# Kernel optimization log

Measured on AMD Instinct MI355X. Metric: run time of the kernel, lower is better.

## Reference

```python
import jax, jax.numpy as jnp
import numpy as np

B, T, C = 4, 2048, 1024


def wkv(k, v, w, u, reverse):
    """RWKV WKV scan with running-max stabilization.
    k, v: [B, T, C]; w, u: [C]. Returns y: [B, T, C]."""
    def step(carry, kv):
        num, den, mx = carry          # each [B, C]
        k_t, v_t = kv                 # each [B, C]
        ku = k_t + u
        m = jnp.maximum(mx, ku)
        e1 = jnp.exp(mx - m)
        e2 = jnp.exp(ku - m)
        y = (e1 * num + e2 * v_t) / (e1 * den + e2)
        # state update with decay w
        mw = mx + w
        mn = jnp.maximum(mw, k_t)
        e1s = jnp.exp(mw - mn)
        e2s = jnp.exp(k_t - mn)
        return (e1s * num + e2s * v_t, e1s * den + e2s, mn), y

    z = jnp.zeros_like(k[:, 0])
    init = (z, z, jnp.full_like(z, -1e38))
    ks = jnp.swapaxes(k, 0, 1)  # [T, B, C]
    vs = jnp.swapaxes(v, 0, 1)
    _, ys = jax.lax.scan(step, init, (ks, vs), reverse=reverse)
    return jnp.swapaxes(ys, 0, 1)


def setup_inputs() -> dict:
    key = jax.random.key(0)
    k1, k2, k3, k4, k5, k6, k7 = jax.random.split(key, 7)
    x = jax.random.normal(k1, (B, T, C), dtype=jnp.float32)
    rkv_w = jax.random.normal(k2, (6 * C, C), dtype=jnp.float32) / np.sqrt(C)
    out_w = jax.random.normal(k3, (C, 2 * C), dtype=jnp.float32) / np.sqrt(2 * C)
    time_decay = jax.random.uniform(k4, (C,), jnp.float32, -6.0, -5.0)
    time_first = jax.random.uniform(k5, (C,), jnp.float32, -3.0, 0.0)
    time_decay_rev = jax.random.uniform(k6, (C,), jnp.float32, -6.0, -5.0)
    time_first_rev = jax.random.uniform(k7, (C,), jnp.float32, -3.0, 0.0)
    return {"x": x, "rkv_w": rkv_w, "out_w": out_w,
            "time_decay": time_decay, "time_first": time_first,
            "time_decay_rev": time_decay_rev, "time_first_rev": time_first_rev}


def reference(x, rkv_w, out_w, time_decay, time_first, time_decay_rev, time_first_rev):
    b, t, c = x.shape
    rkv = jnp.einsum('btc,dc->btd', x, rkv_w).reshape(b, t, 2, 3, c)
    r_f, k_f, v_f = rkv[:, :, 0, 0], rkv[:, :, 0, 1], rkv[:, :, 0, 2]
    r_b, k_b, v_b = rkv[:, :, 1, 0], rkv[:, :, 1, 1], rkv[:, :, 1, 2]
    out_f = jax.nn.sigmoid(r_f) * wkv(k_f, v_f, -jnp.exp(time_decay), time_first, False)
    out_b = jax.nn.sigmoid(r_b) * wkv(k_b, v_b, -jnp.exp(time_decay_rev), time_first_rev, True)
    out_cat = jnp.concatenate([out_f, out_b], axis=-1)  # [B, T, 2C]
    return jnp.einsum('btd,cd->btc', out_cat, out_w)
```

## Files before the change

kernel.cpp:

```cpp
#include <hip/hip_runtime.h>
#include <cstdint>
#include <cstddef>

#define Bdim 4
#define Tdim 2048
#define Cdim 1024

#define SEG  16
#define CHB  32
#define LSEG (Tdim / SEG)

typedef __attribute__((ext_vector_type(8))) short bf16x8;
typedef __attribute__((ext_vector_type(4))) float f32x4;

__device__ __forceinline__ unsigned short f2bf(float f) {
    unsigned int u = __float_as_uint(f);
    u += 0x7fffu + ((u >> 16) & 1u);
    return (unsigned short)(u >> 16);
}
__device__ __forceinline__ float bf2f(unsigned short h) {
    return __uint_as_float((unsigned int)h << 16);
}

__device__ __forceinline__ void gload_lds16(const void* g, void* l) {
    __builtin_amdgcn_global_load_lds(
        (const __attribute__((address_space(1))) unsigned int*)g,
        (__attribute__((address_space(3))) unsigned int*)l,
        16, 0, 0);
}

__global__ __launch_bounds__(256) void cast_f32_bf16(
    const float* __restrict__ in, unsigned short* __restrict__ out, int n4)
{
    int i = blockIdx.x * 256 + threadIdx.x;
    if (i >= n4) return;
    float4 v = ((const float4*)in)[i];
    ushort4 o;
    o.x = f2bf(v.x); o.y = f2bf(v.y); o.z = f2bf(v.z); o.w = f2bf(v.w);
    ((ushort4*)out)[i] = o;
}

__device__ __forceinline__ void stage_half(
    const unsigned short* __restrict__ G, int row0, int K, int elemoff,
    char* slot, int wave, int lane)
{
    const int sl = (lane & 3) ^ ((lane >> 3) & 3);
    const unsigned short* gp = G + (size_t)(row0 + wave * 16 + (lane >> 2)) * K
                                 + elemoff + sl * 8;
    gload_lds16(gp, slot + wave * 1024);
    gload_lds16(gp + (size_t)128 * K, slot + 8192 + wave * 1024);
}

#define GPHASE(D, KH, MH, SG, SROW0, SOFF, SSLOT, VM)                          \
  {                                                                            \
    const char* As_ = ldsb + (D)*32768 + (KH)*16384;                           \
    const char* Bs_ = ldsb + 65536 + (D)*32768 + (KH)*16384;                   \
    bf16x8 a_[4], b_[4];                                                       \
    _Pragma("unroll")                                                          \
    for (int i_ = 0; i_ < 4; ++i_)                                             \
      a_[i_] = *(const bf16x8*)(As_ + (wm*128 + ((MH)*4+i_)*16 + fr)*64 + cswz);\
    _Pragma("unroll")                                                          \
    for (int j_ = 0; j_ < 4; ++j_)                                             \
      b_[j_] = *(const bf16x8*)(Bs_ + (wn*64 + j_*16 + fr)*64 + cswz);         \
    stage_half(SG, SROW0, K, SOFF, SSLOT, wave, lane);                         \
    __builtin_amdgcn_s_barrier();                                              \
    __builtin_amdgcn_sched_barrier(0);                                         \
    __builtin_amdgcn_s_setprio(1);                                             \
    _Pragma("unroll")                                                          \
    for (int i_ = 0; i_ < 4; ++i_)                                             \
      _Pragma("unroll")                                                        \
      for (int j_ = 0; j_ < 4; ++j_)                                           \
        acc[(MH)*4+i_][j_] = __builtin_amdgcn_mfma_f32_16x16x32_bf16(          \
            a_[i_], b_[j_], acc[(MH)*4+i_][j_], 0, 0, 0);                      \
    __builtin_amdgcn_s_setprio(0);                                             \
    if (VM) { asm volatile("s_waitcnt vmcnt(8)" ::: "memory"); }               \
    __builtin_amdgcn_s_barrier();                                              \
    __builtin_amdgcn_sched_barrier(0);                                         \
  }

__global__ __launch_bounds__(512, 2) void gemm_bf16_nt_256_obf(
    const unsigned short* __restrict__ A, const unsigned short* __restrict__ B,
    unsigned short* __restrict__ C, int M, int N, int K, int gx)
{
    __shared__ char ldsbuf[131072];
    char* ldsb = ldsbuf;

    const int tid  = threadIdx.x;
    const int wave = tid >> 6;
    const int lane = tid & 63;
    const int wm = wave >> 2;
    const int wn = wave & 3;
    const int fr = lane & 15;
    const int cswz = (((lane >> 4) ^ ((fr >> 1) & 3)) << 4);

    const int nwg = gridDim.x;
    const int cpx = nwg >> 3;
    const int b0  = blockIdx.x;
    const int swz = (b0 & 7) * cpx + (b0 >> 3);
    const int bx  = swz % gx;
    const int by  = swz / gx;
    const int m0 = by * 256;
    const int n0 = bx * 256;

    const int NKT = K >> 6;
    const int NI  = K >> 7;

    f32x4 acc[8][4] = {};

    stage_half(A, m0, K, 0,  ldsb + 0,             wave, lane);
    stage_half(B, n0, K, 0,  ldsb + 65536,         wave, lane);
    stage_half(A, m0, K, 32, ldsb + 16384,         wave, lane);
    stage_half(B, n0, K, 32, ldsb + 65536 + 16384, wave, lane);
    stage_half(A, m0, K, 64, ldsb + 32768,         wave, lane);
    stage_half(B, n0, K, 64, ldsb + 65536 + 32768, wave, lane);
    asm volatile("s_waitcnt vmcnt(8)" ::: "memory");
    __builtin_amdgcn_s_barrier();
    __builtin_amdgcn_sched_barrier(0);

    for (int i = 0; i < NI; ++i) {
        const int k1e = (2 * i + 1) * 64;
        int k2 = 2 * i + 2; if (k2 >= NKT) k2 = NKT - 1;
        int k3 = 2 * i + 3; if (k3 >= NKT) k3 = NKT - 1;
        const int k2e = k2 * 64, k3e = k3 * 64;

        GPHASE(0, 0, 0, A, m0, k1e + 32, ldsb + 32768 + 16384,         0)
        GPHASE(0, 0, 1, B, n0, k1e + 32, ldsb + 65536 + 32768 + 16384, 1)
        GPHASE(0, 1, 0, A, m0, k2e,      ldsb + 0,                     0)
        GPHASE(0, 1, 1, B, n0, k2e,      ldsb + 65536,                 1)
        GPHASE(1, 0, 0, A, m0, k2e + 32, ldsb + 16384,                 0)
        GPHASE(1, 0, 1, B, n0, k2e + 32, ldsb + 65536 + 16384,         1)
        GPHASE(1, 1, 0, A, m0, k3e,      ldsb + 32768,                 0)
        GPHASE(1, 1, 1, B, n0, k3e,      ldsb + 65536 + 32768,         1)
    }

    #pragma unroll
    for (int mi = 0; mi < 8; ++mi) {
        const int row = m0 + wm * 128 + mi * 16 + (lane >> 4) * 4;
        #pragma unroll
        for (int nj = 0; nj < 4; ++nj) {
            const int col = n0 + wn * 64 + nj * 16 + fr;
            #pragma unroll
            for (int r = 0; r < 4; ++r)
                C[(size_t)(row + r) * N + col] = f2bf(acc[mi][nj][r]);
        }
    }
}

__global__ __launch_bounds__(256) void gemm_bf16_nt(
    const unsigned short* __restrict__ A, const unsigned short* __restrict__ B,
    float* __restrict__ C, int M, int N, int K)
{
    __shared__ unsigned short As[128 * 32];
    __shared__ unsigned short Bs[128 * 32];

    const int tid  = threadIdx.x;
    const int wave = tid >> 6;
    const int lane = tid & 63;
    const int m0 = blockIdx.y * 128;
    const int n0 = blockIdx.x * 128;
    const int wr = wave >> 1, wc = wave & 1;

    const int srow = tid >> 2;
    const int scol = (tid & 3) * 8;
    const unsigned short* Ag = A + (size_t)(m0 + srow) * K + scol;
    const unsigned short* Bg = B + (size_t)(n0 + srow) * K + scol;
    char* AsW = (char*)As + wave * 1024;
    char* BsW = (char*)Bs + wave * 1024;

    f32x4 acc[4][4] = {};

    const int fr = lane & 15;
    const int fk = (lane >> 4) * 8;

    for (int k0 = 0; k0 < K; k0 += 32) {
        gload_lds16(Ag + k0,                  AsW);
        gload_lds16(Ag + k0 + (size_t)64 * K, AsW + 4096);
        gload_lds16(Bg + k0,                  BsW);
        gload_lds16(Bg + k0 + (size_t)64 * K, BsW + 4096);
        __syncthreads();

        bf16x8 af[4], bfr_[4];
        #pragma unroll
        for (int f = 0; f < 4; ++f) {
            af[f]   = *(const bf16x8*)&As[(wr * 64 + f * 16 + fr) * 32 + fk];
            bfr_[f] = *(const bf16x8*)&Bs[(wc * 64 + f * 16 + fr) * 32 + fk];
        }
        #pragma unroll
        for (int i = 0; i < 4; ++i)
            #pragma unroll
            for (int j = 0; j < 4; ++j)
                acc[i][j] = __builtin_amdgcn_mfma_f32_16x16x32_bf16(
                    af[i], bfr_[j], acc[i][j], 0, 0, 0);
        __syncthreads();
    }

    #pragma unroll
    for (int i = 0; i < 4; ++i) {
        const int row = m0 + wr * 64 + i * 16 + (lane >> 4) * 4;
        #pragma unroll
        for (int j = 0; j < 4; ++j) {
            const int col = n0 + wc * 64 + j * 16 + (lane & 15);
            #pragma unroll
            for (int r = 0; r < 4; ++r)
                C[(size_t)(row + r) * N + col] = acc[i][j][r];
        }
    }
}

__global__ __launch_bounds__(512) void wkv_scan_par(
    const unsigned short* __restrict__ rkv,
    const float* __restrict__ td,  const float* __restrict__ tf,
    const float* __restrict__ tdr, const float* __restrict__ tfr,
    unsigned short* __restrict__ outcat)
{
    __shared__ float sBn[SEG][CHB], sBd[SEG][CHB], sMb[SEG][CHB];

    const int tid = threadIdx.x;
    const int ch  = tid & (CHB - 1);
    const int seg = tid >> 5;

    const int bi  = blockIdx.x;
    const int b   = bi >> 6;
    const int rem = bi & 63;
    const int dir = rem >> 5;
    const int c   = (rem & 31) * CHB + ch;

    const float w = -__expf(dir ? tdr[c] : td[c]);
    const float u = dir ? tfr[c] : tf[c];

    const int strideT = 6 * Cdim;
    const int tstep   = dir ? -strideT : strideT;
    const int t0      = dir ? (Tdim - 1 - seg * LSEG) : (seg * LSEG);

    const unsigned short* pbase = rkv + ((size_t)b * Tdim + t0) * strideT + dir * 3 * Cdim + c;

    const int PF = 4;

    float bn = 0.0f, bd = 0.0f, mb = -1e38f;
    {
        const unsigned short* q = pbase;
        float kk[PF], vv[PF];
        #pragma unroll
        for (int i = 0; i < PF; ++i) {
            kk[i] = bf2f(q[Cdim]); vv[i] = bf2f(q[2 * Cdim]); q += tstep;
        }
        for (int t = 0; t < LSEG; t += PF) {
            float kn[PF], vn[PF];
            if (t + PF < LSEG) {
                #pragma unroll
                for (int i = 0; i < PF; ++i) {
                    kn[i] = bf2f(q[Cdim]); vn[i] = bf2f(q[2 * Cdim]); q += tstep;
                }
            }
            #pragma unroll
            for (int i = 0; i < PF; ++i) {
                const float k_ = kk[i], v_ = vv[i];
                const float mw = mb + w;
                const float mn = fmaxf(mw, k_);
                const float e1 = __expf(mw - mn);
                const float e2 = __expf(k_ - mn);
                bn = e1 * bn + e2 * v_;
                bd = e1 * bd + e2;
                mb = mn;
            }
            #pragma unroll
            for (int i = 0; i < PF; ++i) { kk[i] = kn[i]; vv[i] = vn[i]; }
        }
    }
    sBn[seg][ch] = bn; sBd[seg][ch] = bd; sMb[seg][ch] = mb;
    __syncthreads();

    if (tid < CHB) {
        float n = 0.0f, d = 0.0f, m = -1e38f;
        const float a = w * (float)LSEG;
        for (int s = 0; s < SEG; ++s) {
            const float tn = sBn[s][tid], tdn = sBd[s][tid], tm = sMb[s][tid];
            sBn[s][tid] = n; sBd[s][tid] = d; sMb[s][tid] = m;
            const float ma = m + a;
            const float mm = fmaxf(ma, tm);
            const float e1 = __expf(ma - mm);
            const float e2 = __expf(tm - mm);
            n = e1 * n + e2 * tn;
            d = e1 * d + e2 * tdn;
            m = mm;
        }
    }
    __syncthreads();

    float num = sBn[seg][ch], den = sBd[seg][ch], mx = sMb[seg][ch];
    {
        const unsigned short* q = pbase;
        unsigned short* po = outcat + ((size_t)b * Tdim + t0) * (2 * Cdim) + dir * Cdim + c;
        const int ostep = dir ? -(2 * Cdim) : (2 * Cdim);

        float rr[PF], kk[PF], vv[PF];
        #pragma unroll
        for (int i = 0; i < PF; ++i) {
            rr[i] = bf2f(q[0]); kk[i] = bf2f(q[Cdim]); vv[i] = bf2f(q[2 * Cdim]); q += tstep;
        }
        for (int t = 0; t < LSEG; t += PF) {
            float rn[PF], kn[PF], vn[PF];
            if (t + PF < LSEG) {
                #pragma unroll
                for (int i = 0; i < PF; ++i) {
                    rn[i] = bf2f(q[0]); kn[i] = bf2f(q[Cdim]); vn[i] = bf2f(q[2 * Cdim]); q += tstep;
                }
            }
            #pragma unroll
            for (int i = 0; i < PF; ++i) {
                const float k_ = kk[i], v_ = vv[i], r_ = rr[i];
                const float ku = k_ + u;
                const float m  = fmaxf(mx, ku);
                const float e1 = __expf(mx - m);
                const float e2 = __expf(ku - m);
                const float y  = (e1 * num + e2 * v_) / (e1 * den + e2);
                const float sr = 1.0f / (1.0f + __expf(-r_));
                *po = f2bf(sr * y);
                po += ostep;
                const float mw  = mx + w;
                const float mn  = fmaxf(mw, k_);
                const float e1s = __expf(mw - mn);
                const float e2s = __expf(k_ - mn);
                num = e1s * num + e2s * v_;
                den = e1s * den + e2s;
                mx  = mn;
            }
            #pragma unroll
            for (int i = 0; i < PF; ++i) { rr[i] = rn[i]; kk[i] = kn[i]; vv[i] = vn[i]; }
        }
    }
}

extern "C" void kernel_launch(void* const* d_in, const int* in_sizes, int n_in,
                              void* d_out, int out_size, void* d_ws, size_t ws_size,
                              hipStream_t stream)
{
    const float* x    = (const float*)d_in[0];
    const float* rkvw = (const float*)d_in[1];
    const float* outw = (const float*)d_in[2];
    const float* td   = (const float*)d_in[3];
    const float* tf   = (const float*)d_in[4];
    const float* tdr  = (const float*)d_in[5];
    const float* tfr  = (const float*)d_in[6];
    float* out = (float*)d_out;

    const int M = Bdim * Tdim;

    char* ws = (char*)d_ws;
    unsigned short* rkv = (unsigned short*)ws;
    unsigned short* xb  = (unsigned short*)(ws + 100663296);
    unsigned short* wb  = (unsigned short*)(ws + 117440512);
    unsigned short* ob  = (unsigned short*)(ws + 130023424);
    unsigned short* cat = (unsigned short*)(ws + 134217728);

    dim3 blk(256);

    hipLaunchKernelGGL(cast_f32_bf16, dim3((M * Cdim / 4 + 255) / 256), blk, 0, stream,
                       x, xb, M * Cdim / 4);
    hipLaunchKernelGGL(cast_f32_bf16, dim3((6 * Cdim * Cdim / 4 + 255) / 256), blk, 0, stream,
                       rkvw, wb, 6 * Cdim * Cdim / 4);
    hipLaunchKernelGGL(cast_f32_bf16, dim3((Cdim * 2 * Cdim / 4 + 255) / 256), blk, 0, stream,
                       outw, ob, Cdim * 2 * Cdim / 4);

    hipLaunchKernelGGL(gemm_bf16_nt_256_obf, dim3((6 * Cdim / 256) * (M / 256)), dim3(512),
                       0, stream, xb, wb, rkv, M, 6 * Cdim, Cdim, 6 * Cdim / 256);

    hipLaunchKernelGGL(wkv_scan_par, dim3(Bdim * 2 * (Cdim / CHB)), dim3(512), 0, stream,
                       rkv, td, tf, tdr, tfr, cat);

    hipLaunchKernelGGL(gemm_bf16_nt, dim3(Cdim / 128, M / 128), blk, 0, stream,
                       cat, ob, out, M, Cdim, 2 * Cdim);
}
```

Measured before the change: 259.2 us.

## Retile first GEMM to 256x128 triple-buffered pipeline, merge casts, widen scan segments

The first GEMM moves from a 256x256 tile with a 4-slot, 8-phase schedule to a 256x128 tile with a 3-slot ring buffer and K-step 32. This roughly halves LDS use so four workgroups can share a CU instead of two, aiming for more overlap and better load balance. The three cast kernels are merged into one launch. The WKV scan doubles its segment count (32 segments, 1024 threads) and its prefetch depth to expose more parallelism, at the cost of a larger cross-segment combine. Register pressure at 4 waves-per-EU occupancy, and the shallower 3-slot prefetch, could hurt the GEMM.

```diff
diff --git a/kernel.cpp b/kernel.cpp
--- a/kernel.cpp
+++ b/kernel.cpp
@@ -6,9 +6,15 @@
 #define Tdim 2048
 #define Cdim 1024
 
-#define SEG  16
+#define SEG  32
 #define CHB  32
 #define LSEG (Tdim / SEG)
+
+#define G1_K   1024
+#define G1_N   6144
+#define G1_NKT 32
+#define G1_GXT 48
+#define G1_NWG 1536
 
 typedef __attribute__((ext_vector_type(8))) short bf16x8;
 typedef __attribute__((ext_vector_type(4))) float f32x4;
@@ -29,18 +35,24 @@
         16, 0, 0);
 }
 
-__global__ __launch_bounds__(256) void cast_f32_bf16(
-    const float* __restrict__ in, unsigned short* __restrict__ out, int n4)
+__global__ __launch_bounds__(256) void cast_all(
+    const float* __restrict__ x,  unsigned short* __restrict__ xb,  int n1,
+    const float* __restrict__ w1, unsigned short* __restrict__ wb,  int n2,
+    const float* __restrict__ w2, unsigned short* __restrict__ ob,  int n3)
 {
     int i = blockIdx.x * 256 + threadIdx.x;
-    if (i >= n4) return;
+    const float* in; unsigned short* out;
+    if (i < n1)           { in = x;  out = xb; }
+    else if (i < n1 + n2) { in = w1; out = wb; i -= n1; }
+    else if (i < n1 + n2 + n3) { in = w2; out = ob; i -= n1 + n2; }
+    else return;
     float4 v = ((const float4*)in)[i];
     ushort4 o;
     o.x = f2bf(v.x); o.y = f2bf(v.y); o.z = f2bf(v.z); o.w = f2bf(v.w);
     ((ushort4*)out)[i] = o;
 }
 
-__device__ __forceinline__ void stage_half(
+__device__ __forceinline__ void stage_128(
     const unsigned short* __restrict__ G, int row0, int K, int elemoff,
     char* slot, int wave, int lane)
 {
@@ -48,100 +60,87 @@
     const unsigned short* gp = G + (size_t)(row0 + wave * 16 + (lane >> 2)) * K
                                  + elemoff + sl * 8;
     gload_lds16(gp, slot + wave * 1024);
-    gload_lds16(gp + (size_t)128 * K, slot + 8192 + wave * 1024);
-}
-
-#define GPHASE(D, KH, MH, SG, SROW0, SOFF, SSLOT, VM)                          \
-  {                                                                            \
-    const char* As_ = ldsb + (D)*32768 + (KH)*16384;                           \
-    const char* Bs_ = ldsb + 65536 + (D)*32768 + (KH)*16384;                   \
-    bf16x8 a_[4], b_[4];                                                       \
-    _Pragma("unroll")                                                          \
-    for (int i_ = 0; i_ < 4; ++i_)                                             \
-      a_[i_] = *(const bf16x8*)(As_ + (wm*128 + ((MH)*4+i_)*16 + fr)*64 + cswz);\
-    _Pragma("unroll")                                                          \
-    for (int j_ = 0; j_ < 4; ++j_)                                             \
-      b_[j_] = *(const bf16x8*)(Bs_ + (wn*64 + j_*16 + fr)*64 + cswz);         \
-    stage_half(SG, SROW0, K, SOFF, SSLOT, wave, lane);                         \
-    __builtin_amdgcn_s_barrier();                                              \
-    __builtin_amdgcn_sched_barrier(0);                                         \
-    __builtin_amdgcn_s_setprio(1);                                             \
-    _Pragma("unroll")                                                          \
-    for (int i_ = 0; i_ < 4; ++i_)                                             \
-      _Pragma("unroll")                                                        \
-      for (int j_ = 0; j_ < 4; ++j_)                                           \
-        acc[(MH)*4+i_][j_] = __builtin_amdgcn_mfma_f32_16x16x32_bf16(          \
-            a_[i_], b_[j_], acc[(MH)*4+i_][j_], 0, 0, 0);                      \
-    __builtin_amdgcn_s_setprio(0);                                             \
-    if (VM) { asm volatile("s_waitcnt vmcnt(8)" ::: "memory"); }               \
-    __builtin_amdgcn_s_barrier();                                              \
-    __builtin_amdgcn_sched_barrier(0);                                         \
-  }
-
-__global__ __launch_bounds__(512, 2) void gemm_bf16_nt_256_obf(
+}
+
+__global__ __launch_bounds__(512, 4) void gemm1_3slot(
     const unsigned short* __restrict__ A, const unsigned short* __restrict__ B,
-    unsigned short* __restrict__ C, int M, int N, int K, int gx)
-{
-    __shared__ char ldsbuf[131072];
-    char* ldsb = ldsbuf;
+    unsigned short* __restrict__ C)
+{
+    __shared__ char ldsb[73728];
 
     const int tid  = threadIdx.x;
     const int wave = tid >> 6;
     const int lane = tid & 63;
-    const int wm = wave >> 2;
-    const int wn = wave & 3;
+    const int wm = wave >> 1;
+    const int wn = wave & 1;
     const int fr = lane & 15;
     const int cswz = (((lane >> 4) ^ ((fr >> 1) & 3)) << 4);
 
-    const int nwg = gridDim.x;
-    const int cpx = nwg >> 3;
-    const int b0  = blockIdx.x;
-    const int swz = (b0 & 7) * cpx + (b0 >> 3);
-    const int bx  = swz % gx;
-    const int by  = swz / gx;
+    const int swz = (blockIdx.x & 7) * (G1_NWG >> 3) + (blockIdx.x >> 3);
+    const int bx  = swz % G1_GXT;
+    const int by  = swz / G1_GXT;
     const int m0 = by * 256;
-    const int n0 = bx * 256;
-
-    const int NKT = K >> 6;
-    const int NI  = K >> 7;
-
-    f32x4 acc[8][4] = {};
-
-    stage_half(A, m0, K, 0,  ldsb + 0,             wave, lane);
-    stage_half(B, n0, K, 0,  ldsb + 65536,         wave, lane);
-    stage_half(A, m0, K, 32, ldsb + 16384,         wave, lane);
-    stage_half(B, n0, K, 32, ldsb + 65536 + 16384, wave, lane);
-    stage_half(A, m0, K, 64, ldsb + 32768,         wave, lane);
-    stage_half(B, n0, K, 64, ldsb + 65536 + 32768, wave, lane);
-    asm volatile("s_waitcnt vmcnt(8)" ::: "memory");
+    const int n0 = bx * 128;
+
+    f32x4 acc[4][4] = {};
+
+    stage_128(A, m0,       G1_K, 0,  ldsb + 0,            wave, lane);
+    stage_128(A, m0 + 128, G1_K, 0,  ldsb + 8192,         wave, lane);
+    stage_128(B, n0,       G1_K, 0,  ldsb + 49152,        wave, lane);
+    stage_128(A, m0,       G1_K, 32, ldsb + 16384,        wave, lane);
+    stage_128(A, m0 + 128, G1_K, 32, ldsb + 16384 + 8192, wave, lane);
+    stage_128(B, n0,       G1_K, 32, ldsb + 49152 + 8192, wave, lane);
+    asm volatile("s_waitcnt vmcnt(3)" ::: "memory");
     __builtin_amdgcn_s_barrier();
     __builtin_amdgcn_sched_barrier(0);
 
-    for (int i = 0; i < NI; ++i) {
-        const int k1e = (2 * i + 1) * 64;
-        int k2 = 2 * i + 2; if (k2 >= NKT) k2 = NKT - 1;
-        int k3 = 2 * i + 3; if (k3 >= NKT) k3 = NKT - 1;
-        const int k2e = k2 * 64, k3e = k3 * 64;
-
-        GPHASE(0, 0, 0, A, m0, k1e + 32, ldsb + 32768 + 16384,         0)
-        GPHASE(0, 0, 1, B, n0, k1e + 32, ldsb + 65536 + 32768 + 16384, 1)
-        GPHASE(0, 1, 0, A, m0, k2e,      ldsb + 0,                     0)
-        GPHASE(0, 1, 1, B, n0, k2e,      ldsb + 65536,                 1)
-        GPHASE(1, 0, 0, A, m0, k2e + 32, ldsb + 16384,                 0)
-        GPHASE(1, 0, 1, B, n0, k2e + 32, ldsb + 65536 + 16384,         1)
-        GPHASE(1, 1, 0, A, m0, k3e,      ldsb + 32768,                 0)
-        GPHASE(1, 1, 1, B, n0, k3e,      ldsb + 65536 + 32768,         1)
+    int sR = 0;
+    for (int t = 0; t < G1_NKT; ++t) {
+        const int sW = (sR >= 1) ? sR - 1 : 2;
+        int kst = t + 2; if (kst > G1_NKT - 1) kst = G1_NKT - 1;
+        const int keoff = kst * 32;
+
+        const char* Asl = ldsb + sR * 16384;
+        const char* Bsl = ldsb + 49152 + sR * 8192;
+
+        bf16x8 af[4], bq[4];
+        #pragma unroll
+        for (int i_ = 0; i_ < 4; ++i_)
+            af[i_] = *(const bf16x8*)(Asl + (wm * 64 + i_ * 16 + fr) * 64 + cswz);
+        #pragma unroll
+        for (int j_ = 0; j_ < 4; ++j_)
+            bq[j_] = *(const bf16x8*)(Bsl + (wn * 64 + j_ * 16 + fr) * 64 + cswz);
+
+        stage_128(A, m0,       G1_K, keoff, ldsb + sW * 16384,        wave, lane);
+        stage_128(A, m0 + 128, G1_K, keoff, ldsb + sW * 16384 + 8192, wave, lane);
+        stage_128(B, n0,       G1_K, keoff, ldsb + 49152 + sW * 8192, wave, lane);
+
+        __builtin_amdgcn_s_barrier();
+        __builtin_amdgcn_sched_barrier(0);
+        __builtin_amdgcn_s_setprio(1);
+        #pragma unroll
+        for (int i_ = 0; i_ < 4; ++i_)
+            #pragma unroll
+            for (int j_ = 0; j_ < 4; ++j_)
+                acc[i_][j_] = __builtin_amdgcn_mfma_f32_16x16x32_bf16(
+                    af[i_], bq[j_], acc[i_][j_], 0, 0, 0);
+        __builtin_amdgcn_s_setprio(0);
+        asm volatile("s_waitcnt vmcnt(3)" ::: "memory");
+        __builtin_amdgcn_s_barrier();
+        __builtin_amdgcn_sched_barrier(0);
+
+        sR = (sR < 2) ? sR + 1 : 0;
     }
 
     #pragma unroll
-    for (int mi = 0; mi < 8; ++mi) {
-        const int row = m0 + wm * 128 + mi * 16 + (lane >> 4) * 4;
-        #pragma unroll
-        for (int nj = 0; nj < 4; ++nj) {
-            const int col = n0 + wn * 64 + nj * 16 + fr;
+    for (int i_ = 0; i_ < 4; ++i_) {
+        const int row = m0 + wm * 64 + i_ * 16 + (lane >> 4) * 4;
+        #pragma unroll
+        for (int j_ = 0; j_ < 4; ++j_) {
+            const int col = n0 + wn * 64 + j_ * 16 + fr;
             #pragma unroll
             for (int r = 0; r < 4; ++r)
-                C[(size_t)(row + r) * N + col] = f2bf(acc[mi][nj][r]);
+                C[(size_t)(row + r) * G1_N + col] = f2bf(acc[i_][j_][r]);
         }
     }
 }
@@ -207,7 +206,7 @@
     }
 }
 
-__global__ __launch_bounds__(512) void wkv_scan_par(
+__global__ __launch_bounds__(1024) void wkv_scan_par(
     const unsigned short* __restrict__ rkv,
     const float* __restrict__ td,  const float* __restrict__ tf,
     const float* __restrict__ tdr, const float* __restrict__ tfr,
@@ -234,7 +233,7 @@
 
     const unsigned short* pbase = rkv + ((size_t)b * Tdim + t0) * strideT + dir * 3 * Cdim + c;
 
-    const int PF = 4;
+    const int PF = 8;
 
     float bn = 0.0f, bd = 0.0f, mb = -1e38f;
     {
@@ -353,21 +352,18 @@
     unsigned short* ob  = (unsigned short*)(ws + 130023424);
     unsigned short* cat = (unsigned short*)(ws + 134217728);
 
-    dim3 blk(256);
-
-    hipLaunchKernelGGL(cast_f32_bf16, dim3((M * Cdim / 4 + 255) / 256), blk, 0, stream,
-                       x, xb, M * Cdim / 4);
-    hipLaunchKernelGGL(cast_f32_bf16, dim3((6 * Cdim * Cdim / 4 + 255) / 256), blk, 0, stream,
-                       rkvw, wb, 6 * Cdim * Cdim / 4);
-    hipLaunchKernelGGL(cast_f32_bf16, dim3((Cdim * 2 * Cdim / 4 + 255) / 256), blk, 0, stream,
-                       outw, ob, Cdim * 2 * Cdim / 4);
-
-    hipLaunchKernelGGL(gemm_bf16_nt_256_obf, dim3((6 * Cdim / 256) * (M / 256)), dim3(512),
-                       0, stream, xb, wb, rkv, M, 6 * Cdim, Cdim, 6 * Cdim / 256);
-
-    hipLaunchKernelGGL(wkv_scan_par, dim3(Bdim * 2 * (Cdim / CHB)), dim3(512), 0, stream,
+    const int n1 = M * Cdim / 4;
+    const int n2 = 6 * Cdim * Cdim / 4;
+    const int n3 = Cdim * 2 * Cdim / 4;
+
+    hipLaunchKernelGGL(cast_all, dim3((n1 + n2 + n3 + 255) / 256), dim3(256), 0, stream,
+                       x, xb, n1, rkvw, wb, n2, outw, ob, n3);
+
+    hipLaunchKernelGGL(gemm1_3slot, dim3(G1_NWG), dim3(512), 0, stream, xb, wb, rkv);
+
+    hipLaunchKernelGGL(wkv_scan_par, dim3(Bdim * 2 * (Cdim / CHB)), dim3(1024), 0, stream,
                        rkv, td, tf, tdr, tfr, cat);
 
-    hipLaunchKernelGGL(gemm_bf16_nt, dim3(Cdim / 128, M / 128), blk, 0, stream,
+    hipLaunchKernelGGL(gemm_bf16_nt, dim3(Cdim / 128, M / 128), dim3(256), 0, stream,
                        cat, ob, out, M, Cdim, 2 * Cdim);
 }
```

Measured after the change: 259.9 us. No clear change (+0.3%).
